# Optimization experiments

Measured on AMD Instinct MI355X. Metric: run time of the kernel, lower is better.

Reference implementation:

```python
import jax, jax.numpy as jnp
import numpy as np


def setup_inputs() -> dict:
    key = jax.random.key(0)
    k1, k2, k3 = jax.random.split(key, 3)
    B, N, D = 16, 2048, 128
    q = jax.random.normal(k1, (B, N, D), dtype=jnp.float32)
    k = jax.random.normal(k2, (B, D, N), dtype=jnp.float32)
    v = jax.random.normal(k3, (B, N, D), dtype=jnp.float32)
    return {"q": q, "k": k, "v": v}


def reference(q, k, v):
    # scores: [B, N, N] — note NO 1/sqrt(d) scaling, matching the source
    scores = jnp.einsum('bnd,bdm->bnm', q, k)
    probs = jax.nn.softmax(scores, axis=-1)
    out = jnp.einsum('bnm,bmd->bnd', probs, v)  # [B, N, D]
    return out
```

## Files before the change

kernel.cpp:

```cpp
#include <hip/hip_runtime.h>


typedef __attribute__((ext_vector_type(8))) _Float16 f16x8;
typedef __attribute__((ext_vector_type(16))) float f32x16;
typedef __attribute__((ext_vector_type(2))) uint u32x2;

constexpr int Bz = 16;
constexpr int Nn = 2048;
constexpr int Dd = 128;
constexpr int BM = 128;
constexpr int BN = 32;

__device__ __forceinline__ int swz(int r) { return (r ^ (r >> 3)) & 7; }
__device__ __forceinline__ int sw4(int d) { return ((d >> 1) ^ (d >> 3)) & 3; }

__device__ __forceinline__ uint pkrtz(float a, float b) {
    return __builtin_bit_cast(uint, __builtin_amdgcn_cvt_pkrtz(a, b));
}

__device__ __forceinline__ float exp2i(float x) {
    return __builtin_amdgcn_exp2f(x);
}

__global__ __launch_bounds__(512, 2)
void fattn_kernel(const float* __restrict__ qg,
                  const float* __restrict__ kg,
                  const float* __restrict__ vg,
                  float* __restrict__ og)
{
    __shared__ ushort lds_k[2][BN * Dd];
    __shared__ ushort lds_v[2][Dd * BN];

    const int bid  = blockIdx.x;
    const int xcd  = bid & 7;
    const int idx  = bid >> 3;
    const int b    = xcd * 2 + (idx >> 4);
    const int q0   = (idx & 15) * BM;
    const int tid  = threadIdx.x;
    const int wv   = tid >> 6;
    const int lane = tid & 63;
    const int h    = lane >> 5;
    const int l31  = lane & 31;
    const bool producer = (wv >= 4);

    const int ptid = (wv - 4) * 64 + lane;
    const int g8  = ptid & 7;
    const int g32 = ptid >> 3;
    const float* kbase = kg + (size_t)b * Dd * Nn;
    const float* vbase = vg + (size_t)b * Nn * Dd;
    float4 kr0[4], vr0[4], kr1[4], vr1[4];

    auto issue_loads = [&](int n0, float4 (&kr)[4], float4 (&vr)[4]) {
        const float* s0 = kbase + (size_t)(g32 * 4) * Nn + n0 + g8 * 4;
        kr[0] = *(const float4*)(s0);
        kr[1] = *(const float4*)(s0 + Nn);
        kr[2] = *(const float4*)(s0 + 2 * Nn);
        kr[3] = *(const float4*)(s0 + 3 * Nn);
        const float* t0 = vbase + (size_t)(n0 + g8 * 4) * Dd + g32 * 4;
        vr[0] = *(const float4*)(t0);
        vr[1] = *(const float4*)(t0 + Dd);
        vr[2] = *(const float4*)(t0 + 2 * Dd);
        vr[3] = *(const float4*)(t0 + 3 * Dd);
    };
    auto write_lds = [&](int buf, const float4 (&kr)[4], const float4 (&vr)[4]) {
        u32x2* kw2 = (u32x2*)lds_k[buf];
        const float* k0 = (const float*)&kr[0];
        const float* k1 = (const float*)&kr[1];
        const float* k2 = (const float*)&kr[2];
        const float* k3 = (const float*)&kr[3];
        #pragma unroll
        for (int j = 0; j < 4; ++j) {
            const int n = g8 * 4 + j;
            u32x2 pv;
            pv[0] = pkrtz(k0[j], k1[j]);
            pv[1] = pkrtz(k2[j], k3[j]);
            kw2[n * 32 + (g32 ^ (swz(n) << 1) ^ (n & 8))] = pv;
        }
        u32x2* vw2 = (u32x2*)lds_v[buf];
        const float* v0 = (const float*)&vr[0];
        const float* v1 = (const float*)&vr[1];
        const float* v2 = (const float*)&vr[2];
        const float* v3 = (const float*)&vr[3];
        #pragma unroll
        for (int j = 0; j < 4; ++j) {
            const int d = g32 * 4 + j;
            const int rowp = d ^ ((d >> 5) & 1);
            u32x2 pv;
            pv[0] = pkrtz(v0[j], v1[j]);
            pv[1] = pkrtz(v2[j], v3[j]);
            vw2[rowp * 8 + (g8 ^ (sw4(d) << 1))] = pv;
        }
    };

    f16x8 qf[8];
    if (!producer) {
        const float* qp = qg + (size_t)(b * Nn + q0 + wv * 32 + l31) * Dd + h * 8;
        #pragma unroll
        for (int c = 0; c < 8; ++c) {
            float4 x0 = *(const float4*)(qp + c * 16);
            float4 x1 = *(const float4*)(qp + c * 16 + 4);
            const float xv[8] = {x0.x, x0.y, x0.z, x0.w, x1.x, x1.y, x1.z, x1.w};
            union { f16x8 v; _Float16 e[8]; } u;
            #pragma unroll
            for (int j = 0; j < 8; ++j)
                u.e[j] = (_Float16)(xv[j] * 1.44269504088896340736f);
            qf[c] = u.v;
        }
    }
    f32x16 accO[4];
    #pragma unroll
    for (int dt = 0; dt < 4; ++dt)
        #pragma unroll
        for (int r = 0; r < 16; ++r) accO[dt][r] = 0.f;
    float m_i = -1e30f, l_i = 0.f;

    auto consume = [&](const ushort* kb, const ushort* vb) {
        f32x16 accS, accT;
        #pragma unroll
        for (int r = 0; r < 16; ++r) { accS[r] = 0.f; accT[r] = 0.f; }
        {
            const int sw = swz(l31) << 3;
            const int rx = (l31 & 8) << 2;
            __builtin_amdgcn_s_setprio(1);
            #pragma unroll
            for (int c = 0; c < 4; ++c) {
                f16x8 kf0 = *(const f16x8*)&kb[l31 * Dd + (((2 * c) * 16 + h * 8) ^ sw ^ rx)];
                f16x8 kf1 = *(const f16x8*)&kb[l31 * Dd + (((2 * c + 1) * 16 + h * 8) ^ sw ^ rx)];
                accS = __builtin_amdgcn_mfma_f32_32x32x16_f16(kf0, qf[2 * c],     accS, 0, 0, 0);
                accT = __builtin_amdgcn_mfma_f32_32x32x16_f16(kf1, qf[2 * c + 1], accT, 0, 0, 0);
            }
            __builtin_amdgcn_s_setprio(0);
        }
        #pragma unroll
        for (int r = 0; r < 16; ++r) accS[r] += accT[r];

        f16x8 vf[4][2];
        #pragma unroll
        for (int dt = 0; dt < 4; ++dt) {
            const int drow = dt * 32 + l31;
            const int rowp = drow ^ ((drow >> 5) & 1);
            const int sv = sw4(drow) << 3;
            vf[dt][0] = *(const f16x8*)&vb[rowp * BN + ((8 * h) ^ sv)];
            vf[dt][1] = *(const f16x8*)&vb[rowp * BN + ((16 + 8 * h) ^ sv)];
        }

        float t0 = fmaxf(accS[0], accS[1]),  t1 = fmaxf(accS[2], accS[3]);
        float t2 = fmaxf(accS[4], accS[5]),  t3 = fmaxf(accS[6], accS[7]);
        float t4 = fmaxf(accS[8], accS[9]),  t5 = fmaxf(accS[10], accS[11]);
        float t6 = fmaxf(accS[12], accS[13]), t7 = fmaxf(accS[14], accS[15]);
        float u0 = fmaxf(t0, t1), u1 = fmaxf(t2, t3);
        float u2 = fmaxf(t4, t5), u3 = fmaxf(t6, t7);
        float mx = fmaxf(fmaxf(u0, u1), fmaxf(u2, u3));
        mx = fmaxf(mx, __shfl_xor(mx, 32, 64));

        if (!__all(mx <= m_i + 8.f)) {
            const float mn = fmaxf(m_i, mx);
            const float al = exp2i(m_i - mn);
            m_i = mn;
            l_i *= al;
            #pragma unroll
            for (int dt = 0; dt < 4; ++dt)
                #pragma unroll
                for (int r = 0; r < 16; ++r) accO[dt][r] *= al;
        }
        #pragma unroll
        for (int r = 0; r < 16; ++r) accS[r] = exp2i(accS[r] - m_i);
        {
            float a0 = accS[0] + accS[1],   a1 = accS[2] + accS[3];
            float a2 = accS[4] + accS[5],   a3 = accS[6] + accS[7];
            float a4 = accS[8] + accS[9],   a5 = accS[10] + accS[11];
            float a6 = accS[12] + accS[13], a7 = accS[14] + accS[15];
            float b0 = a0 + a1, b1 = a2 + a3, b2 = a4 + a5, b3 = a6 + a7;
            l_i += (b0 + b1) + (b2 + b3);
        }

        const uint pA0 = pkrtz(accS[0],  accS[1]);
        const uint pA1 = pkrtz(accS[2],  accS[3]);
        const uint pB0 = pkrtz(accS[4],  accS[5]);
        const uint pB1 = pkrtz(accS[6],  accS[7]);
        const uint pC0 = pkrtz(accS[8],  accS[9]);
        const uint pC1 = pkrtz(accS[10], accS[11]);
        const uint pD0 = pkrtz(accS[12], accS[13]);
        const uint pD1 = pkrtz(accS[14], accS[15]);
        const uint yA0 = __shfl_xor(pA0, 32, 64);
        const uint yA1 = __shfl_xor(pA1, 32, 64);
        const uint yB0 = __shfl_xor(pB0, 32, 64);
        const uint yB1 = __shfl_xor(pB1, 32, 64);
        const uint yC0 = __shfl_xor(pC0, 32, 64);
        const uint yC1 = __shfl_xor(pC1, 32, 64);
        const uint yD0 = __shfl_xor(pD0, 32, 64);
        const uint yD1 = __shfl_xor(pD1, 32, 64);
        union { uint u[4]; f16x8 v; } P0, P1;
        P0.u[0] = h ? yB0 : pA0;
        P0.u[1] = h ? yB1 : pA1;
        P0.u[2] = h ? pB0 : yA0;
        P0.u[3] = h ? pB1 : yA1;
        P1.u[0] = h ? yD0 : pC0;
        P1.u[1] = h ? yD1 : pC1;
        P1.u[2] = h ? pD0 : yC0;
        P1.u[3] = h ? pD1 : yC1;
        const f16x8 pf0 = P0.v, pf1 = P1.v;

        __builtin_amdgcn_s_setprio(1);
        #pragma unroll
        for (int dt = 0; dt < 4; ++dt) {
            accO[dt] = __builtin_amdgcn_mfma_f32_32x32x16_f16(vf[dt][0], pf0, accO[dt], 0, 0, 0);
            accO[dt] = __builtin_amdgcn_mfma_f32_32x32x16_f16(vf[dt][1], pf1, accO[dt], 0, 0, 0);
        }
        __builtin_amdgcn_s_setprio(0);
    };

    if (producer) {
        issue_loads(0,  kr0, vr0);
        issue_loads(BN, kr1, vr1);
        write_lds(0, kr0, vr0);
    }
    __syncthreads();

    constexpr int ITERS = Nn / BN;
    for (int it = 0; it < ITERS; it += 2) {
        if (producer) {
            write_lds(1, kr1, vr1);
            if (it + 2 < ITERS) issue_loads((it + 2) * BN, kr0, vr0);
        } else {
            consume(lds_k[0], lds_v[0]);
        }
        __syncthreads();
        if (producer) {
            if (it + 2 < ITERS) write_lds(0, kr0, vr0);
            if (it + 3 < ITERS) issue_loads((it + 3) * BN, kr1, vr1);
        } else {
            consume(lds_k[1], lds_v[1]);
        }
        __syncthreads();
    }

    if (!producer) {
        float l = l_i + __shfl_xor(l_i, 32, 64);
        const float inv = 1.f / l;
        float* ob = og + (size_t)(b * Nn + q0 + wv * 32 + l31) * Dd;
        #pragma unroll
        for (int dt = 0; dt < 4; ++dt) {
            #pragma unroll
            for (int g = 0; g < 4; ++g) {
                float4 val;
                val.x = accO[dt][4 * g + 0] * inv;
                val.y = accO[dt][4 * g + 1] * inv;
                val.z = accO[dt][4 * g + 2] * inv;
                val.w = accO[dt][4 * g + 3] * inv;
                *(float4*)(ob + dt * 32 + 8 * g + 4 * h) = val;
            }
        }
    }
}

extern "C" void kernel_launch(void* const* d_in, const int* in_sizes, int n_in,
                              void* d_out, int out_size, void* d_ws, size_t ws_size,
                              hipStream_t stream) {
    const float* q = (const float*)d_in[0];
    const float* k = (const float*)d_in[1];
    const float* v = (const float*)d_in[2];
    float* o = (float*)d_out;
    (void)d_ws; (void)ws_size; (void)in_sizes; (void)n_in; (void)out_size;
    fattn_kernel<<<dim3(Bz * (Nn / BM)), dim3(512), 0, stream>>>(q, k, v, o);
}
```

Measured before the change: 135.6 us.

## Halve query tile to 64 rows with 256-thread blocks and single-buffered producer registers

```diff
diff --git a/kernel.cpp b/kernel.cpp
--- a/kernel.cpp
+++ b/kernel.cpp
@@ -8,7 +8,7 @@
 constexpr int Bz = 16;
 constexpr int Nn = 2048;
 constexpr int Dd = 128;
-constexpr int BM = 128;
+constexpr int BM = 64;
 constexpr int BN = 32;
 
 __device__ __forceinline__ int swz(int r) { return (r ^ (r >> 3)) & 7; }
@@ -22,7 +22,7 @@
     return __builtin_amdgcn_exp2f(x);
 }
 
-__global__ __launch_bounds__(512, 2)
+__global__ __launch_bounds__(256, 2)
 void fattn_kernel(const float* __restrict__ qg,
                   const float* __restrict__ kg,
                   const float* __restrict__ vg,
@@ -34,61 +34,59 @@
     const int bid  = blockIdx.x;
     const int xcd  = bid & 7;
     const int idx  = bid >> 3;
-    const int b    = xcd * 2 + (idx >> 4);
-    const int q0   = (idx & 15) * BM;
+    const int b    = xcd * 2 + (idx >> 5);
+    const int q0   = (idx & 31) * BM;
     const int tid  = threadIdx.x;
     const int wv   = tid >> 6;
     const int lane = tid & 63;
     const int h    = lane >> 5;
     const int l31  = lane & 31;
-    const bool producer = (wv >= 4);
-
-    const int ptid = (wv - 4) * 64 + lane;
-    const int g8  = ptid & 7;
-    const int g32 = ptid >> 3;
+    const bool producer = (wv >= 2);
+
+    const int ptid = (wv - 2) * 64 + lane;
+    const int k8 = ptid >> 3;
+    const int kc = ptid & 7;
+    const int v4 = ptid >> 5;
+    const int vc = ptid & 31;
     const float* kbase = kg + (size_t)b * Dd * Nn;
     const float* vbase = vg + (size_t)b * Nn * Dd;
-    float4 kr0[4], vr0[4], kr1[4], vr1[4];
-
-    auto issue_loads = [&](int n0, float4 (&kr)[4], float4 (&vr)[4]) {
-        const float* s0 = kbase + (size_t)(g32 * 4) * Nn + n0 + g8 * 4;
-        kr[0] = *(const float4*)(s0);
-        kr[1] = *(const float4*)(s0 + Nn);
-        kr[2] = *(const float4*)(s0 + 2 * Nn);
-        kr[3] = *(const float4*)(s0 + 3 * Nn);
-        const float* t0 = vbase + (size_t)(n0 + g8 * 4) * Dd + g32 * 4;
-        vr[0] = *(const float4*)(t0);
-        vr[1] = *(const float4*)(t0 + Dd);
-        vr[2] = *(const float4*)(t0 + 2 * Dd);
-        vr[3] = *(const float4*)(t0 + 3 * Dd);
+    float4 kr[8], vr[8];
+
+    auto issue_loads = [&](int n0) {
+        const float* s0 = kbase + (size_t)(k8 * 8) * Nn + n0 + kc * 4;
+        #pragma unroll
+        for (int j = 0; j < 8; ++j) kr[j] = *(const float4*)(s0 + (size_t)j * Nn);
+        const float* t0 = vbase + (size_t)(n0 + v4 * 8) * Dd + vc * 4;
+        #pragma unroll
+        for (int j = 0; j < 8; ++j) vr[j] = *(const float4*)(t0 + (size_t)j * Dd);
     };
-    auto write_lds = [&](int buf, const float4 (&kr)[4], const float4 (&vr)[4]) {
+    auto write_lds = [&](int buf) {
         u32x2* kw2 = (u32x2*)lds_k[buf];
-        const float* k0 = (const float*)&kr[0];
-        const float* k1 = (const float*)&kr[1];
-        const float* k2 = (const float*)&kr[2];
-        const float* k3 = (const float*)&kr[3];
         #pragma unroll
         for (int j = 0; j < 4; ++j) {
-            const int n = g8 * 4 + j;
-            u32x2 pv;
-            pv[0] = pkrtz(k0[j], k1[j]);
-            pv[1] = pkrtz(k2[j], k3[j]);
-            kw2[n * 32 + (g32 ^ (swz(n) << 1) ^ (n & 8))] = pv;
+            const int n = kc * 4 + j;
+            const int sx = (swz(n) << 1) ^ (n & 8);
+            u32x2 p0, p1;
+            p0[0] = pkrtz(((const float*)&kr[0])[j], ((const float*)&kr[1])[j]);
+            p0[1] = pkrtz(((const float*)&kr[2])[j], ((const float*)&kr[3])[j]);
+            p1[0] = pkrtz(((const float*)&kr[4])[j], ((const float*)&kr[5])[j]);
+            p1[1] = pkrtz(((const float*)&kr[6])[j], ((const float*)&kr[7])[j]);
+            kw2[n * 32 + ((2 * k8)     ^ sx)] = p0;
+            kw2[n * 32 + ((2 * k8 + 1) ^ sx)] = p1;
         }
         u32x2* vw2 = (u32x2*)lds_v[buf];
-        const float* v0 = (const float*)&vr[0];
-        const float* v1 = (const float*)&vr[1];
-        const float* v2 = (const float*)&vr[2];
-        const float* v3 = (const float*)&vr[3];
         #pragma unroll
         for (int j = 0; j < 4; ++j) {
-            const int d = g32 * 4 + j;
+            const int d = vc * 4 + j;
             const int rowp = d ^ ((d >> 5) & 1);
-            u32x2 pv;
-            pv[0] = pkrtz(v0[j], v1[j]);
-            pv[1] = pkrtz(v2[j], v3[j]);
-            vw2[rowp * 8 + (g8 ^ (sw4(d) << 1))] = pv;
+            const int sx = sw4(d) << 1;
+            u32x2 p0, p1;
+            p0[0] = pkrtz(((const float*)&vr[0])[j], ((const float*)&vr[1])[j]);
+            p0[1] = pkrtz(((const float*)&vr[2])[j], ((const float*)&vr[3])[j]);
+            p1[0] = pkrtz(((const float*)&vr[4])[j], ((const float*)&vr[5])[j]);
+            p1[1] = pkrtz(((const float*)&vr[6])[j], ((const float*)&vr[7])[j]);
+            vw2[rowp * 8 + ((2 * v4)     ^ sx)] = p0;
+            vw2[rowp * 8 + ((2 * v4 + 1) ^ sx)] = p1;
         }
     };
 
@@ -115,24 +113,20 @@
     float m_i = -1e30f, l_i = 0.f;
 
     auto consume = [&](const ushort* kb, const ushort* vb) {
-        f32x16 accS, accT;
-        #pragma unroll
-        for (int r = 0; r < 16; ++r) { accS[r] = 0.f; accT[r] = 0.f; }
+        f32x16 accS;
+        #pragma unroll
+        for (int r = 0; r < 16; ++r) accS[r] = 0.f;
         {
             const int sw = swz(l31) << 3;
             const int rx = (l31 & 8) << 2;
             __builtin_amdgcn_s_setprio(1);
             #pragma unroll
-            for (int c = 0; c < 4; ++c) {
-                f16x8 kf0 = *(const f16x8*)&kb[l31 * Dd + (((2 * c) * 16 + h * 8) ^ sw ^ rx)];
-                f16x8 kf1 = *(const f16x8*)&kb[l31 * Dd + (((2 * c + 1) * 16 + h * 8) ^ sw ^ rx)];
-                accS = __builtin_amdgcn_mfma_f32_32x32x16_f16(kf0, qf[2 * c],     accS, 0, 0, 0);
-                accT = __builtin_amdgcn_mfma_f32_32x32x16_f16(kf1, qf[2 * c + 1], accT, 0, 0, 0);
+            for (int c = 0; c < 8; ++c) {
+                f16x8 kf = *(const f16x8*)&kb[l31 * Dd + ((c * 16 + h * 8) ^ sw ^ rx)];
+                accS = __builtin_amdgcn_mfma_f32_32x32x16_f16(kf, qf[c], accS, 0, 0, 0);
             }
             __builtin_amdgcn_s_setprio(0);
         }
-        #pragma unroll
-        for (int r = 0; r < 16; ++r) accS[r] += accT[r];
 
         f16x8 vf[4][2];
         #pragma unroll
@@ -211,24 +205,24 @@
     };
 
     if (producer) {
-        issue_loads(0,  kr0, vr0);
-        issue_loads(BN, kr1, vr1);
-        write_lds(0, kr0, vr0);
+        issue_loads(0);
+        write_lds(0);
+        issue_loads(BN);
     }
     __syncthreads();
 
     constexpr int ITERS = Nn / BN;
     for (int it = 0; it < ITERS; it += 2) {
         if (producer) {
-            write_lds(1, kr1, vr1);
-            if (it + 2 < ITERS) issue_loads((it + 2) * BN, kr0, vr0);
+            write_lds(1);
+            if (it + 2 < ITERS) issue_loads((it + 2) * BN);
         } else {
             consume(lds_k[0], lds_v[0]);
         }
         __syncthreads();
         if (producer) {
-            if (it + 2 < ITERS) write_lds(0, kr0, vr0);
-            if (it + 3 < ITERS) issue_loads((it + 3) * BN, kr1, vr1);
+            if (it + 2 < ITERS) write_lds(0);
+            if (it + 3 < ITERS) issue_loads((it + 3) * BN);
         } else {
             consume(lds_k[1], lds_v[1]);
         }
@@ -262,5 +256,5 @@
     const float* v = (const float*)d_in[2];
     float* o = (float*)d_out;
     (void)d_ws; (void)ws_size; (void)in_sizes; (void)n_in; (void)out_size;
-    fattn_kernel<<<dim3(Bz * (Nn / BM)), dim3(512), 0, stream>>>(q, k, v, o);
-}
+    fattn_kernel<<<dim3(Bz * (Nn / BM)), dim3(256), 0, stream>>>(q, k, v, o);
+}
```

After: 157.1 us. +15.8%, slower.
